# Kernel optimization log

Hardware: AMD Instinct MI355X
Metric: run time of the kernel (lower is better)

The kernel has to match this reference:

```python
import jax, jax.numpy as jnp
import numpy as np

B, N, C, H = 2, 2048, 1024, 16
D = C // H  # head_dim = 64


def _rope_freqs(n, d_half, theta=10000.0):
    inv = 1.0 / (theta ** (np.arange(0, d_half, dtype=np.float32) / d_half))
    ang = np.arange(n, dtype=np.float32)[:, None] * inv[None, :]
    return jnp.asarray(np.cos(ang)), jnp.asarray(np.sin(ang))


def setup_inputs() -> dict:
    key = jax.random.key(0)
    ks = jax.random.split(key, 5)
    cos, sin = _rope_freqs(N, D // 2)
    s = 0.02
    return {
        "x": jax.random.normal(ks[0], (B, N, C), jnp.float32),
        "w_qkv": jax.random.normal(ks[1], (3 * C, C), jnp.float32) * s,
        "b_qkv": jnp.zeros((3 * C,), jnp.float32),
        "w_proj": jax.random.normal(ks[2], (C, C), jnp.float32) * s,
        "b_proj": jnp.zeros((C,), jnp.float32),
        "freqs_cos": cos,
        "freqs_sin": sin,
    }


def _apply_rope(t, cos, sin):
    # t: (B, H, N, D); consecutive pairs (even, odd) form complex numbers,
    # matching torch.view_as_complex on reshape(..., D//2, 2).
    te = t[..., 0::2]
    to = t[..., 1::2]
    cos = cos[None, None, :, :]  # (1,1,N,D//2)
    sin = sin[None, None, :, :]
    oe = te * cos - to * sin
    oo = te * sin + to * cos
    return jnp.stack([oe, oo], axis=-1).reshape(t.shape)


def reference(x, w_qkv, b_qkv, w_proj, b_proj, freqs_cos, freqs_sin):
    b, n, c = x.shape
    qkv = x @ w_qkv.T + b_qkv                      # (B,N,3C)
    qkv = qkv.reshape(b, n, 3, H, D).transpose(2, 0, 3, 1, 4)  # (3,B,H,N,D)
    q, k, v = qkv[0], qkv[1], qkv[2]
    q = _apply_rope(q, freqs_cos, freqs_sin)
    k = _apply_rope(k, freqs_cos, freqs_sin)
    scale = 1.0 / jnp.sqrt(jnp.asarray(D, x.dtype))
    scores = jnp.einsum("bhqd,bhkd->bhqk", q, k) * scale
    attn = jax.nn.softmax(scores, axis=-1)
    out = jnp.einsum("bhqk,bhkd->bhqd", attn, v)   # (B,H,N,D)
    out = out.transpose(0, 2, 1, 3).reshape(b, n, c)
    return out @ w_proj.T + b_proj
```

## Files before the change

kernel.cpp:

```cpp
#include <hip/hip_runtime.h>
#include <hip/hip_bf16.h>
#include <stdint.h>

#define BB 2
#define NN 2048
#define CC 1024
#define HH 16
#define DD 64
#define C3 3072

typedef __attribute__((ext_vector_type(8))) short bf16x8;
typedef __attribute__((ext_vector_type(4))) float f32x4;
typedef __attribute__((ext_vector_type(4))) unsigned short ushort4_t;

__device__ __forceinline__ unsigned short f2bf(float f) {
  union { float f; unsigned u; } v; v.f = f;
  unsigned r = v.u + 0x7FFFu + ((v.u >> 16) & 1u);
  return (unsigned short)(r >> 16);
}

#if __has_builtin(__builtin_amdgcn_exp2f)
#define EXP2(x) __builtin_amdgcn_exp2f(x)
#else
#define EXP2(x) exp2f(x)
#endif

#define QSCALE 0.18033688f

#define GLDS(g, l) __builtin_amdgcn_global_load_lds( \
    (const __attribute__((address_space(1))) void*)(g), \
    (__attribute__((address_space(3))) void*)(l), 16, 0, 0)

__global__ __launch_bounds__(256) void k_cvt(
    const float* __restrict__ x, const float* __restrict__ wq,
    const float* __restrict__ wp,
    unsigned short* __restrict__ xb, unsigned short* __restrict__ wqb,
    unsigned short* __restrict__ wpb)
{
  int blk = blockIdx.x;
  const float* s; unsigned short* d; int i;
  if (blk < 4096)      { s = x;  d = xb;  i = blk * 256 + threadIdx.x; }
  else if (blk < 7168) { s = wq; d = wqb; i = (blk - 4096) * 256 + threadIdx.x; }
  else                 { s = wp; d = wpb; i = (blk - 7168) * 256 + threadIdx.x; }
  float4 v = ((const float4*)s)[i];
  ushort4_t o;
  o.x = f2bf(v.x); o.y = f2bf(v.y); o.z = f2bf(v.z); o.w = f2bf(v.w);
  ((ushort4_t*)d)[i] = o;
}

__global__ __launch_bounds__(256) void k_gemm_qkv(
    const unsigned short* __restrict__ A, const unsigned short* __restrict__ Bt,
    const float* __restrict__ bias,
    const float* __restrict__ cosb, const float* __restrict__ sinb,
    unsigned short* __restrict__ Qg, unsigned short* __restrict__ Kg,
    unsigned short* __restrict__ Vnd)
{
  __shared__ __align__(16) unsigned short As[128 * 64];
  __shared__ __align__(16) unsigned short Bs[128 * 64];
  const int tid  = threadIdx.x;
  const int lane = tid & 63;
  const int wave = tid >> 6;
  const int bm = blockIdx.y * 128;
  const int bn = blockIdx.x * 128;
  const int wm = (wave >> 1) * 64;
  const int wn = (wave & 1) * 64;
  const int frow   = lane & 15;
  const int fchunk = lane >> 4;
  const int K = 1024;

  f32x4 acc[4][4] = {};

  const int srow[4] = { tid >> 3, 32 + (tid >> 3), 64 + (tid >> 3), 96 + (tid >> 3) };
  int scol[4];
#pragma unroll
  for (int j = 0; j < 4; ++j) scol[j] = ((tid & 7) ^ (srow[j] & 7)) * 8;

  for (int k0 = 0; k0 < K; k0 += 64) {
#pragma unroll
    for (int j = 0; j < 4; ++j) {
      GLDS(A  + (size_t)(bm + srow[j]) * K + k0 + scol[j], As + (size_t)(j * 256 + tid) * 8);
      GLDS(Bt + (size_t)(bn + srow[j]) * K + k0 + scol[j], Bs + (size_t)(j * 256 + tid) * 8);
    }
    __syncthreads();

#pragma unroll
    for (int kh = 0; kh < 2; ++kh) {
      bf16x8 af[4], bfr[4];
#pragma unroll
      for (int t = 0; t < 4; ++t) {
        int ra = wm + t * 16 + frow;
        int rb = wn + t * 16 + frow;
        af[t]  = *(const bf16x8*)(As + ra * 64 + (((kh * 4 + fchunk) ^ (ra & 7)) << 3));
        bfr[t] = *(const bf16x8*)(Bs + rb * 64 + (((kh * 4 + fchunk) ^ (rb & 7)) << 3));
      }
#pragma unroll
      for (int mt = 0; mt < 4; ++mt)
#pragma unroll
        for (int nt = 0; nt < 4; ++nt)
          acc[mt][nt] = __builtin_amdgcn_mfma_f32_16x16x32_bf16(af[mt], bfr[nt], acc[mt][nt], 0, 0, 0);
    }
    __syncthreads();
  }

  const int er0  = (lane >> 4) * 4;
  const int ecol = lane & 15;
  const int region = bn >> 10;
  unsigned short* dstQK = (region == 0) ? Qg : Kg;

#pragma unroll
  for (int nt = 0; nt < 4; ++nt) {
    const int col = bn + wn + nt * 16 + ecol;
    const float bv = bias[col];
    const int c64 = (wn + nt * 16 + ecol) & 63;
    const int h   = (col >> 6) & 15;
    const int ii  = c64 >> 1;
#pragma unroll
    for (int mt = 0; mt < 4; ++mt)
#pragma unroll
      for (int r = 0; r < 4; ++r) {
        const int rowg = bm + wm + mt * 16 + er0 + r;
        const int b = rowg >> 11, n = rowg & (NN - 1);
        float v = acc[mt][nt][r] + bv;
        float vp = __shfl_xor(v, 1, 64);
        const size_t o = ((size_t)(b * HH + h) * NN + n) * DD + c64;
        if (region == 2) {
          Vnd[o] = f2bf(v);
        } else {
          float cth = cosb[n * 32 + ii], sth = sinb[n * 32 + ii];
          float ov = (c64 & 1) ? (vp * sth + v * cth)
                               : (v * cth - vp * sth);
          if (region == 0) ov *= QSCALE;
          dstQK[o] = f2bf(ov);
        }
      }
  }
}

__global__ __launch_bounds__(256) void k_vt(
    const unsigned short* __restrict__ Vnd, unsigned short* __restrict__ Vt)
{
  __shared__ unsigned short t[64][66];
  const int tid = threadIdx.x;
  const int bh = blockIdx.x >> 5;
  const int n0 = (blockIdx.x & 31) * 64;

  const unsigned short* src = Vnd + ((size_t)bh * NN + n0) * DD;
  const int nl = tid >> 2, d0 = (tid & 3) * 16;
#pragma unroll
  for (int j = 0; j < 4; ++j) {
    ushort4_t v = *(const ushort4_t*)(src + (size_t)nl * DD + d0 + j * 4);
    t[nl][d0 + j * 4 + 0] = v.x;
    t[nl][d0 + j * 4 + 1] = v.y;
    t[nl][d0 + j * 4 + 2] = v.z;
    t[nl][d0 + j * 4 + 3] = v.w;
  }
  __syncthreads();
  const int d = tid >> 2, m0 = (tid & 3) * 16;
  unsigned short* dst = Vt + ((size_t)bh * DD + d) * NN + n0 + m0;
#pragma unroll
  for (int j = 0; j < 4; ++j) {
    ushort4_t o;
    o.x = t[m0 + j * 4 + 0][d];
    o.y = t[m0 + j * 4 + 1][d];
    o.z = t[m0 + j * 4 + 2][d];
    o.w = t[m0 + j * 4 + 3][d];
    *(ushort4_t*)(dst + j * 4) = o;
  }
}

__global__ __launch_bounds__(256) void k_attn(
    const unsigned short* __restrict__ Qg, const unsigned short* __restrict__ Kg,
    const unsigned short* __restrict__ Vtg,
    float* __restrict__ Op, float* __restrict__ lp)
{
  __shared__ __align__(16) unsigned short Ks[2][64 * 64];
  __shared__ __align__(16) unsigned short Vs[2][64 * 64];
  __shared__ __align__(16) unsigned short Ps[4][32 * 32];

  const int tid  = threadIdx.x;
  const int lane = tid & 63;
  const int wave = tid >> 6;
  const int blk  = blockIdx.x;
  const int bh   = blk >> 5;
  const int qt   = (blk >> 1) & 15;
  const int half = blk & 1;
  const int q0 = qt * 128 + wave * 32;
  const int frow   = lane & 15;
  const int fchunk = lane >> 4;
  const int er0  = (lane >> 4) * 4;
  const int ecol = lane & 15;

  const unsigned short* Qb = Qg  + (size_t)bh * NN * DD;
  const unsigned short* Kb = Kg  + (size_t)bh * NN * DD;
  const unsigned short* Vb = Vtg + (size_t)bh * DD * NN;
  const int jbase = half * (NN / 2);

  bf16x8 qf[2][2];
#pragma unroll
  for (int m = 0; m < 2; ++m)
#pragma unroll
    for (int kt = 0; kt < 2; ++kt)
      qf[m][kt] = *(const bf16x8*)(Qb + (size_t)(q0 + m * 16 + frow) * DD + kt * 32 + fchunk * 8);

  bf16x8 ones;
#pragma unroll
  for (int i = 0; i < 8; ++i) ones[i] = (short)0x3F80;

  f32x4 oacc[2][4] = {};
  f32x4 lacc[2] = {};

  const int row0 = tid >> 3, cc0 = tid & 7;
  const int sw0 = (cc0 ^ (row0 & 7)) * 8;

  GLDS(Kb + (size_t)(jbase + row0) * DD + sw0,      Ks[0] + (size_t)tid * 8);
  GLDS(Vb + (size_t)row0 * NN + jbase + sw0,        Vs[0] + (size_t)tid * 8);
  GLDS(Kb + (size_t)(jbase + row0 + 32) * DD + sw0, Ks[0] + (size_t)(tid + 256) * 8);
  GLDS(Vb + (size_t)(row0 + 32) * NN + jbase + sw0, Vs[0] + (size_t)(tid + 256) * 8);

  for (int t = 0; t < NN / 128; ++t) {
    const int p = t & 1;
    __syncthreads();

    if (t + 1 < NN / 128) {
      const int j = jbase + (t + 1) * 64;
      GLDS(Kb + (size_t)(j + row0) * DD + sw0,      Ks[1 - p] + (size_t)tid * 8);
      GLDS(Vb + (size_t)row0 * NN + j + sw0,        Vs[1 - p] + (size_t)tid * 8);
      GLDS(Kb + (size_t)(j + row0 + 32) * DD + sw0, Ks[1 - p] + (size_t)(tid + 256) * 8);
      GLDS(Vb + (size_t)(row0 + 32) * NN + j + sw0, Vs[1 - p] + (size_t)(tid + 256) * 8);
    }

    f32x4 sacc[2][4] = {};
#pragma unroll
    for (int nt = 0; nt < 4; ++nt) {
      int kr = nt * 16 + frow;
      bf16x8 kf0 = *(const bf16x8*)(Ks[p] + kr * 64 + ((fchunk       ^ (kr & 7)) << 3));
      bf16x8 kf1 = *(const bf16x8*)(Ks[p] + kr * 64 + (((fchunk + 4) ^ (kr & 7)) << 3));
#pragma unroll
      for (int m = 0; m < 2; ++m) {
        sacc[m][nt] = __builtin_amdgcn_mfma_f32_16x16x32_bf16(qf[m][0], kf0, sacc[m][nt], 0, 0, 0);
        sacc[m][nt] = __builtin_amdgcn_mfma_f32_16x16x32_bf16(qf[m][1], kf1, sacc[m][nt], 0, 0, 0);
      }
    }

#pragma unroll
    for (int kh = 0; kh < 2; ++kh) {
#pragma unroll
      for (int m = 0; m < 2; ++m)
#pragma unroll
        for (int r = 0; r < 4; ++r) {
          int prow = m * 16 + er0 + r;
#pragma unroll
          for (int nh = 0; nh < 2; ++nh) {
            float pv = EXP2(sacc[m][kh * 2 + nh][r]);
            union { float f; unsigned u; } cv; cv.f = pv;
            int cl = nh * 16 + ecol;
            Ps[wave][prow * 32 + (((cl >> 3) ^ (prow & 3)) << 3) + (cl & 7)] =
                (unsigned short)(cv.u >> 16);
          }
        }

      bf16x8 pf[2];
#pragma unroll
      for (int m = 0; m < 2; ++m) {
        int pr = m * 16 + frow;
        pf[m] = *(const bf16x8*)(&Ps[wave][pr * 32 + ((fchunk ^ (pr & 3)) << 3)]);
        lacc[m] = __builtin_amdgcn_mfma_f32_16x16x32_bf16(pf[m], ones, lacc[m], 0, 0, 0);
      }
#pragma unroll
      for (int dt = 0; dt < 4; ++dt) {
        int vr = dt * 16 + frow;
        bf16x8 vf = *(const bf16x8*)(Vs[p] + vr * 64 + (((kh * 4 + fchunk) ^ (vr & 7)) << 3));
#pragma unroll
        for (int m = 0; m < 2; ++m)
          oacc[m][dt] = __builtin_amdgcn_mfma_f32_16x16x32_bf16(pf[m], vf, oacc[m][dt], 0, 0, 0);
      }
    }
  }

  float* Oh = Op + (size_t)half * (32u * NN * DD);
#pragma unroll
  for (int m = 0; m < 2; ++m) {
#pragma unroll
    for (int dt = 0; dt < 4; ++dt)
#pragma unroll
      for (int r = 0; r < 4; ++r) {
        int qrow = q0 + m * 16 + er0 + r;
        int d = dt * 16 + ecol;
        Oh[((size_t)bh * NN + qrow) * DD + d] = oacc[m][dt][r];
      }
    if (ecol == 0) {
#pragma unroll
      for (int r = 0; r < 4; ++r) {
        int qrow = q0 + m * 16 + er0 + r;
        lp[(size_t)half * (32 * NN) + bh * NN + qrow] = lacc[m][r];
      }
    }
  }
}

__global__ __launch_bounds__(256) void k_combine(
    const float* __restrict__ Op, const float* __restrict__ lp,
    unsigned short* __restrict__ aob)
{
  int idx = blockIdx.x * 256 + threadIdx.x;
  int q  = idx >> 4;
  int d4 = (idx & 15) * 4;
  const float4 a = *(const float4*)(Op + (size_t)q * DD + d4);
  const float4 b = *(const float4*)(Op + (size_t)(32u * NN * DD) + (size_t)q * DD + d4);
  float inv = 1.0f / (lp[q] + lp[32 * NN + q]);
  int bh = q >> 11, n = q & (NN - 1);
  int bb = bh >> 4, h = bh & 15;
  ushort4_t o;
  o.x = f2bf((a.x + b.x) * inv);
  o.y = f2bf((a.y + b.y) * inv);
  o.z = f2bf((a.z + b.z) * inv);
  o.w = f2bf((a.w + b.w) * inv);
  *(ushort4_t*)(aob + ((size_t)(bb * NN + n) * CC) + h * DD + d4) = o;
}

__global__ __launch_bounds__(256) void k_gemm_proj(
    const unsigned short* __restrict__ A, const unsigned short* __restrict__ Bt,
    const float* __restrict__ bias, float* __restrict__ Co)
{
  __shared__ __align__(16) unsigned short As[64 * 64];
  __shared__ __align__(16) unsigned short Bs[128 * 64];
  const int tid  = threadIdx.x;
  const int lane = tid & 63;
  const int wave = tid >> 6;
  const int bm = blockIdx.y * 64;
  const int bn = blockIdx.x * 128;
  const int wm = (wave >> 1) * 32;
  const int wn = (wave & 1) * 64;
  const int frow   = lane & 15;
  const int fchunk = lane >> 4;
  const int K = 1024;

  f32x4 acc[2][4] = {};

  const int r0 = tid >> 3;
  const int sc0 = ((tid & 7) ^ (r0 & 7)) * 8;
  const int r1 = 32 + r0;
  const int sc1 = ((tid & 7) ^ (r1 & 7)) * 8;

  for (int k0 = 0; k0 < K; k0 += 64) {
    GLDS(A + (size_t)(bm + r0) * K + k0 + sc0, As + (size_t)tid * 8);
    GLDS(A + (size_t)(bm + r1) * K + k0 + sc1, As + (size_t)(tid + 256) * 8);
#pragma unroll
    for (int j = 0; j < 4; ++j) {
      int rb = j * 32 + r0;
      int scb = ((tid & 7) ^ (rb & 7)) * 8;
      GLDS(Bt + (size_t)(bn + rb) * K + k0 + scb, Bs + (size_t)(j * 256 + tid) * 8);
    }
    __syncthreads();

#pragma unroll
    for (int kh = 0; kh < 2; ++kh) {
      bf16x8 af[2], bfr[4];
#pragma unroll
      for (int t = 0; t < 2; ++t) {
        int ra = wm + t * 16 + frow;
        af[t] = *(const bf16x8*)(As + ra * 64 + (((kh * 4 + fchunk) ^ (ra & 7)) << 3));
      }
#pragma unroll
      for (int t = 0; t < 4; ++t) {
        int rb = wn + t * 16 + frow;
        bfr[t] = *(const bf16x8*)(Bs + rb * 64 + (((kh * 4 + fchunk) ^ (rb & 7)) << 3));
      }
#pragma unroll
      for (int mt = 0; mt < 2; ++mt)
#pragma unroll
        for (int nt = 0; nt < 4; ++nt)
          acc[mt][nt] = __builtin_amdgcn_mfma_f32_16x16x32_bf16(af[mt], bfr[nt], acc[mt][nt], 0, 0, 0);
    }
    __syncthreads();
  }

  const int er0  = (lane >> 4) * 4;
  const int ecol = lane & 15;
#pragma unroll
  for (int nt = 0; nt < 4; ++nt) {
    int col = bn + wn + nt * 16 + ecol;
    float bv = bias[col];
#pragma unroll
    for (int mt = 0; mt < 2; ++mt)
#pragma unroll
      for (int r = 0; r < 4; ++r) {
        int rowg = bm + wm + mt * 16 + er0 + r;
        Co[(size_t)rowg * CC + col] = acc[mt][nt][r] + bv;
      }
  }
}

extern "C" void kernel_launch(void* const* d_in, const int* in_sizes, int n_in,
                              void* d_out, int out_size, void* d_ws, size_t ws_size,
                              hipStream_t stream)
{
  const float* x      = (const float*)d_in[0];
  const float* w_qkv  = (const float*)d_in[1];
  const float* b_qkv  = (const float*)d_in[2];
  const float* w_proj = (const float*)d_in[3];
  const float* b_proj = (const float*)d_in[4];
  const float* fcos   = (const float*)d_in[5];
  const float* fsin   = (const float*)d_in[6];
  float* out = (float*)d_out;

  char* ws = (char*)d_ws;
  unsigned short* xb     = (unsigned short*)(ws);
  unsigned short* wqkvb  = (unsigned short*)(ws + 8388608);
  unsigned short* wprojb = (unsigned short*)(ws + 14680064);
  unsigned short* Qb     = (unsigned short*)(ws + 16777216);
  unsigned short* Kb     = (unsigned short*)(ws + 25165824);
  unsigned short* Vnd    = (unsigned short*)(ws + 33554432);
  unsigned short* Vtb    = (unsigned short*)(ws + 41943040);
  unsigned short* aob    = (unsigned short*)(ws + 50331648);
  float*          Op     = (float*)(ws + 58720256);
  float*          lp     = (float*)(ws + 92274688);

  k_cvt<<<8192, 256, 0, stream>>>(x, w_qkv, w_proj, xb, wqkvb, wprojb);

  k_gemm_qkv<<<dim3(24, 32), 256, 0, stream>>>(xb, wqkvb, b_qkv, fcos, fsin,
                                               Qb, Kb, Vnd);
  k_vt<<<1024, 256, 0, stream>>>(Vnd, Vtb);

  k_attn<<<1024, 256, 0, stream>>>(Qb, Kb, Vtb, Op, lp);
  k_combine<<<4096, 256, 0, stream>>>(Op, lp, aob);

  k_gemm_proj<<<dim3(8, 64), 256, 0, stream>>>(aob, wprojb, b_proj, out);
}
```

Measured before the change: 237.7 us.

## Fuse V transpose into QKV GEMM epilogue via LDS staging, shrink K tile

```diff
diff --git a/kernel.cpp b/kernel.cpp
--- a/kernel.cpp
+++ b/kernel.cpp
@@ -53,10 +53,11 @@
     const float* __restrict__ bias,
     const float* __restrict__ cosb, const float* __restrict__ sinb,
     unsigned short* __restrict__ Qg, unsigned short* __restrict__ Kg,
-    unsigned short* __restrict__ Vnd)
-{
-  __shared__ __align__(16) unsigned short As[128 * 64];
-  __shared__ __align__(16) unsigned short Bs[128 * 64];
+    unsigned short* __restrict__ Vt)
+{
+  __shared__ __align__(16) unsigned short Sh[16384];
+  unsigned short* As = Sh;
+  unsigned short* Bs = Sh + 4096;
   const int tid  = threadIdx.x;
   const int lane = tid & 63;
   const int wave = tid >> 6;
@@ -64,107 +65,89 @@
   const int bn = blockIdx.x * 128;
   const int wm = (wave >> 1) * 64;
   const int wn = (wave & 1) * 64;
-  const int frow   = lane & 15;
-  const int fchunk = lane >> 4;
+  const int frow = lane & 15;
+  const int fk   = (lane >> 4) * 8;
   const int K = 1024;
 
   f32x4 acc[4][4] = {};
 
-  const int srow[4] = { tid >> 3, 32 + (tid >> 3), 64 + (tid >> 3), 96 + (tid >> 3) };
-  int scol[4];
-#pragma unroll
-  for (int j = 0; j < 4; ++j) scol[j] = ((tid & 7) ^ (srow[j] & 7)) * 8;
-
-  for (int k0 = 0; k0 < K; k0 += 64) {
-#pragma unroll
-    for (int j = 0; j < 4; ++j) {
-      GLDS(A  + (size_t)(bm + srow[j]) * K + k0 + scol[j], As + (size_t)(j * 256 + tid) * 8);
-      GLDS(Bt + (size_t)(bn + srow[j]) * K + k0 + scol[j], Bs + (size_t)(j * 256 + tid) * 8);
-    }
-    __syncthreads();
-
-#pragma unroll
-    for (int kh = 0; kh < 2; ++kh) {
-      bf16x8 af[4], bfr[4];
-#pragma unroll
-      for (int t = 0; t < 4; ++t) {
-        int ra = wm + t * 16 + frow;
-        int rb = wn + t * 16 + frow;
-        af[t]  = *(const bf16x8*)(As + ra * 64 + (((kh * 4 + fchunk) ^ (ra & 7)) << 3));
-        bfr[t] = *(const bf16x8*)(Bs + rb * 64 + (((kh * 4 + fchunk) ^ (rb & 7)) << 3));
-      }
-#pragma unroll
-      for (int mt = 0; mt < 4; ++mt)
-#pragma unroll
-        for (int nt = 0; nt < 4; ++nt)
-          acc[mt][nt] = __builtin_amdgcn_mfma_f32_16x16x32_bf16(af[mt], bfr[nt], acc[mt][nt], 0, 0, 0);
-    }
+  const int row0 = tid >> 2, cc0 = tid & 3;
+  const int row1 = row0 + 64;
+
+  for (int k0 = 0; k0 < K; k0 += 32) {
+    GLDS(A  + (size_t)(bm + row0) * K + k0 + cc0 * 8, As + (size_t)tid * 8);
+    GLDS(Bt + (size_t)(bn + row0) * K + k0 + cc0 * 8, Bs + (size_t)tid * 8);
+    GLDS(A  + (size_t)(bm + row1) * K + k0 + cc0 * 8, As + (size_t)(tid + 256) * 8);
+    GLDS(Bt + (size_t)(bn + row1) * K + k0 + cc0 * 8, Bs + (size_t)(tid + 256) * 8);
+    __syncthreads();
+
+    bf16x8 af[4], bfr[4];
+#pragma unroll
+    for (int t = 0; t < 4; ++t) {
+      af[t]  = *(const bf16x8*)(As + (wm + t * 16 + frow) * 32 + fk);
+      bfr[t] = *(const bf16x8*)(Bs + (wn + t * 16 + frow) * 32 + fk);
+    }
+#pragma unroll
+    for (int mt = 0; mt < 4; ++mt)
+#pragma unroll
+      for (int nt = 0; nt < 4; ++nt)
+        acc[mt][nt] = __builtin_amdgcn_mfma_f32_16x16x32_bf16(af[mt], bfr[nt], acc[mt][nt], 0, 0, 0);
     __syncthreads();
   }
 
   const int er0  = (lane >> 4) * 4;
   const int ecol = lane & 15;
   const int region = bn >> 10;
-  unsigned short* dstQK = (region == 0) ? Qg : Kg;
+  const int gcol0 = bn + wn;
+  const int h  = (gcol0 >> 6) & 15;
+  const int rowg0 = bm + wm;
+  const int b  = rowg0 >> 11;
+  const int n0 = rowg0 & (NN - 1);
+  unsigned short* wt = Sh + wave * 4096;
 
 #pragma unroll
   for (int nt = 0; nt < 4; ++nt) {
-    const int col = bn + wn + nt * 16 + ecol;
-    const float bv = bias[col];
-    const int c64 = (wn + nt * 16 + ecol) & 63;
-    const int h   = (col >> 6) & 15;
+    const int c64 = nt * 16 + ecol;
+    const float bv = bias[gcol0 + c64];
     const int ii  = c64 >> 1;
 #pragma unroll
     for (int mt = 0; mt < 4; ++mt)
 #pragma unroll
       for (int r = 0; r < 4; ++r) {
-        const int rowg = bm + wm + mt * 16 + er0 + r;
-        const int b = rowg >> 11, n = rowg & (NN - 1);
+        const int ml = mt * 16 + er0 + r;
+        const int n  = n0 + ml;
         float v = acc[mt][nt][r] + bv;
         float vp = __shfl_xor(v, 1, 64);
-        const size_t o = ((size_t)(b * HH + h) * NN + n) * DD + c64;
         if (region == 2) {
-          Vnd[o] = f2bf(v);
+          wt[c64 * 64 + ((((ml >> 3) ^ (c64 & 7)) << 3) | (ml & 7))] = f2bf(v);
         } else {
           float cth = cosb[n * 32 + ii], sth = sinb[n * 32 + ii];
           float ov = (c64 & 1) ? (vp * sth + v * cth)
                                : (v * cth - vp * sth);
           if (region == 0) ov *= QSCALE;
-          dstQK[o] = f2bf(ov);
+          wt[ml * 64 + ((((c64 >> 3) ^ (ml & 7)) << 3) | (c64 & 7))] = f2bf(ov);
         }
       }
   }
-}
-
-__global__ __launch_bounds__(256) void k_vt(
-    const unsigned short* __restrict__ Vnd, unsigned short* __restrict__ Vt)
-{
-  __shared__ unsigned short t[64][66];
-  const int tid = threadIdx.x;
-  const int bh = blockIdx.x >> 5;
-  const int n0 = (blockIdx.x & 31) * 64;
-
-  const unsigned short* src = Vnd + ((size_t)bh * NN + n0) * DD;
-  const int nl = tid >> 2, d0 = (tid & 3) * 16;
-#pragma unroll
-  for (int j = 0; j < 4; ++j) {
-    ushort4_t v = *(const ushort4_t*)(src + (size_t)nl * DD + d0 + j * 4);
-    t[nl][d0 + j * 4 + 0] = v.x;
-    t[nl][d0 + j * 4 + 1] = v.y;
-    t[nl][d0 + j * 4 + 2] = v.z;
-    t[nl][d0 + j * 4 + 3] = v.w;
-  }
-  __syncthreads();
-  const int d = tid >> 2, m0 = (tid & 3) * 16;
-  unsigned short* dst = Vt + ((size_t)bh * DD + d) * NN + n0 + m0;
-#pragma unroll
-  for (int j = 0; j < 4; ++j) {
-    ushort4_t o;
-    o.x = t[m0 + j * 4 + 0][d];
-    o.y = t[m0 + j * 4 + 1][d];
-    o.z = t[m0 + j * 4 + 2][d];
-    o.w = t[m0 + j * 4 + 3][d];
-    *(ushort4_t*)(dst + j * 4) = o;
+
+  const int rr = lane >> 3, cc = lane & 7;
+  if (region == 2) {
+    unsigned short* dst = Vt + (size_t)(b * HH + h) * DD * NN + n0;
+#pragma unroll
+    for (int it = 0; it < 8; ++it) {
+      int dl = it * 8 + rr;
+      bf16x8 vv = *(const bf16x8*)(wt + dl * 64 + ((cc ^ (dl & 7)) << 3));
+      *(bf16x8*)(dst + (size_t)dl * NN + cc * 8) = vv;
+    }
+  } else {
+    unsigned short* dqk = ((region == 0) ? Qg : Kg) +
+                          ((size_t)(b * HH + h) * NN + n0) * DD;
+#pragma unroll
+    for (int it = 0; it < 8; ++it) {
+      int ml = it * 8 + rr;
+      bf16x8 vv = *(const bf16x8*)(wt + ml * 64 + ((cc ^ (ml & 7)) << 3));
+      *(bf16x8*)(dqk + (size_t)ml * DD + cc * 8) = vv;
+    }
   }
 }
 
@@ -322,8 +305,8 @@
     const unsigned short* __restrict__ A, const unsigned short* __restrict__ Bt,
     const float* __restrict__ bias, float* __restrict__ Co)
 {
-  __shared__ __align__(16) unsigned short As[64 * 64];
-  __shared__ __align__(16) unsigned short Bs[128 * 64];
+  __shared__ __align__(16) unsigned short As[64 * 32];
+  __shared__ __align__(16) unsigned short Bs[128 * 32];
   const int tid  = threadIdx.x;
   const int lane = tid & 63;
   const int wave = tid >> 6;
@@ -331,47 +314,32 @@
   const int bn = blockIdx.x * 128;
   const int wm = (wave >> 1) * 32;
   const int wn = (wave & 1) * 64;
-  const int frow   = lane & 15;
-  const int fchunk = lane >> 4;
+  const int frow = lane & 15;
+  const int fk   = (lane >> 4) * 8;
   const int K = 1024;
 
   f32x4 acc[2][4] = {};
 
-  const int r0 = tid >> 3;
-  const int sc0 = ((tid & 7) ^ (r0 & 7)) * 8;
-  const int r1 = 32 + r0;
-  const int sc1 = ((tid & 7) ^ (r1 & 7)) * 8;
-
-  for (int k0 = 0; k0 < K; k0 += 64) {
-    GLDS(A + (size_t)(bm + r0) * K + k0 + sc0, As + (size_t)tid * 8);
-    GLDS(A + (size_t)(bm + r1) * K + k0 + sc1, As + (size_t)(tid + 256) * 8);
-#pragma unroll
-    for (int j = 0; j < 4; ++j) {
-      int rb = j * 32 + r0;
-      int scb = ((tid & 7) ^ (rb & 7)) * 8;
-      GLDS(Bt + (size_t)(bn + rb) * K + k0 + scb, Bs + (size_t)(j * 256 + tid) * 8);
-    }
-    __syncthreads();
-
-#pragma unroll
-    for (int kh = 0; kh < 2; ++kh) {
-      bf16x8 af[2], bfr[4];
-#pragma unroll
-      for (int t = 0; t < 2; ++t) {
-        int ra = wm + t * 16 + frow;
-        af[t] = *(const bf16x8*)(As + ra * 64 + (((kh * 4 + fchunk) ^ (ra & 7)) << 3));
-      }
-#pragma unroll
-      for (int t = 0; t < 4; ++t) {
-        int rb = wn + t * 16 + frow;
-        bfr[t] = *(const bf16x8*)(Bs + rb * 64 + (((kh * 4 + fchunk) ^ (rb & 7)) << 3));
-      }
-#pragma unroll
-      for (int mt = 0; mt < 2; ++mt)
-#pragma unroll
-        for (int nt = 0; nt < 4; ++nt)
-          acc[mt][nt] = __builtin_amdgcn_mfma_f32_16x16x32_bf16(af[mt], bfr[nt], acc[mt][nt], 0, 0, 0);
-    }
+  const int row0 = tid >> 2, cc0 = tid & 3;
+
+  for (int k0 = 0; k0 < K; k0 += 32) {
+    GLDS(A  + (size_t)(bm + row0) * K + k0 + cc0 * 8, As + (size_t)tid * 8);
+    GLDS(Bt + (size_t)(bn + row0) * K + k0 + cc0 * 8, Bs + (size_t)tid * 8);
+    GLDS(Bt + (size_t)(bn + row0 + 64) * K + k0 + cc0 * 8, Bs + (size_t)(tid + 256) * 8);
+    __syncthreads();
+
+    bf16x8 af[2], bfr[4];
+#pragma unroll
+    for (int t = 0; t < 2; ++t)
+      af[t] = *(const bf16x8*)(As + (wm + t * 16 + frow) * 32 + fk);
+#pragma unroll
+    for (int t = 0; t < 4; ++t)
+      bfr[t] = *(const bf16x8*)(Bs + (wn + t * 16 + frow) * 32 + fk);
+#pragma unroll
+    for (int mt = 0; mt < 2; ++mt)
+#pragma unroll
+      for (int nt = 0; nt < 4; ++nt)
+        acc[mt][nt] = __builtin_amdgcn_mfma_f32_16x16x32_bf16(af[mt], bfr[nt], acc[mt][nt], 0, 0, 0);
     __syncthreads();
   }
 
@@ -410,7 +378,6 @@
   unsigned short* wprojb = (unsigned short*)(ws + 14680064);
   unsigned short* Qb     = (unsigned short*)(ws + 16777216);
   unsigned short* Kb     = (unsigned short*)(ws + 25165824);
-  unsigned short* Vnd    = (unsigned short*)(ws + 33554432);
   unsigned short* Vtb    = (unsigned short*)(ws + 41943040);
   unsigned short* aob    = (unsigned short*)(ws + 50331648);
   float*          Op     = (float*)(ws + 58720256);
@@ -419,8 +386,7 @@
   k_cvt<<<8192, 256, 0, stream>>>(x, w_qkv, w_proj, xb, wqkvb, wprojb);
 
   k_gemm_qkv<<<dim3(24, 32), 256, 0, stream>>>(xb, wqkvb, b_qkv, fcos, fsin,
-                                               Qb, Kb, Vnd);
-  k_vt<<<1024, 256, 0, stream>>>(Vnd, Vtb);
+                                               Qb, Kb, Vtb);
 
   k_attn<<<1024, 256, 0, stream>>>(Qb, Kb, Vtb, Op, lp);
   k_combine<<<4096, 256, 0, stream>>>(Op, lp, aob);
```

Measured after the change: 239.5 us. Within noise of the previous version (+0.8%).
